# Kernel tuning notes

Hardware: AMD Instinct MI355X
Metric: run time of the kernel (lower is better)

Reference implementation:

```python
import jax, jax.numpy as jnp
import numpy as np

NEG_SLOPE = 0.2  # PyG GATConv default


def setup_inputs() -> dict:
    key = jax.random.key(0)
    k1, k2, k3, k4, k5, k6 = jax.random.split(key, 6)
    N, F_in, F_out, E = 50000, 512, 256, 400000
    x = jax.random.normal(k1, (N, F_in), dtype=jnp.float32)
    adj = jax.random.randint(k2, (2, E), 0, N, dtype=jnp.int64)  # [2, E] edge_index (src, dst)
    glorot = lambda k, shape: jax.random.uniform(
        k, shape, jnp.float32, -1.0, 1.0) * np.sqrt(6.0 / (shape[0] + shape[-1]))
    W = glorot(k3, (F_in, F_out))
    att_src = glorot(k4, (F_out,))
    att_dst = glorot(k5, (F_out,))
    bias = jnp.zeros((F_out,), dtype=jnp.float32)
    return {"x": x, "adj": adj, "W": W, "att_src": att_src, "att_dst": att_dst, "bias": bias}


def reference(x, adj, W, att_src, att_dst, bias):
    N = x.shape[0]
    # add self loops (PyG GATConv default add_self_loops=True)
    loops = jnp.arange(N, dtype=adj.dtype)
    src = jnp.concatenate([adj[0], loops])
    dst = jnp.concatenate([adj[1], loops])

    h = x @ W                          # [N, F_out] projected features
    a_src = h @ att_src                # [N] per-node source attention term
    a_dst = h @ att_dst                # [N]
    e = a_src[src] + a_dst[dst]        # [E+N] edge logits
    e = jnp.where(e > 0, e, NEG_SLOPE * e)  # leaky_relu

    # per-destination softmax over incoming edges (numerically stable)
    m = jax.ops.segment_max(e, dst, num_segments=N)
    ex = jnp.exp(e - m[dst])
    denom = jax.ops.segment_sum(ex, dst, num_segments=N)
    alpha = ex / denom[dst]            # [E+N]

    # weighted scatter-aggregate of source messages
    out = jax.ops.segment_sum(alpha[:, None] * h[src], dst, num_segments=N)
    out = out + bias
    return jax.nn.relu(out)
```

## Files before the change

### kernel.cpp

```cpp
#include <hip/hip_runtime.h>
#include <hip/hip_bf16.h>

typedef __attribute__((ext_vector_type(8))) short bf16x8;
typedef __attribute__((ext_vector_type(4))) float f32x4;
typedef unsigned short u16;

#define F_IN 512
#define F_OUT 256
#define NEG_SLOPE 0.2f
#define LSTRIDE 40

__device__ __forceinline__ float leaky(float e) { return e > 0.f ? e : NEG_SLOPE * e; }

__device__ __forceinline__ u16 f2bf(float x) {
    __hip_bfloat16 h = __float2bfloat16(x);
    return *reinterpret_cast<u16*>(&h);
}
__device__ __forceinline__ void bf2x2(unsigned p, float& a, float& b) {
    a = __uint_as_float(p << 16);
    b = __uint_as_float(p & 0xffff0000u);
}

__device__ __forceinline__ unsigned f2o(float f) {
    unsigned u = __float_as_uint(f);
    return (u & 0x80000000u) ? ~u : (u | 0x80000000u);
}
__device__ __forceinline__ float o2f(unsigned u) {
    return (u & 0x80000000u) ? __uint_as_float(u & 0x7fffffffu) : __uint_as_float(~u);
}

__global__ void k_transpose(const float* __restrict__ W, u16* __restrict__ Wt) {
    int t = blockIdx.x * 256 + threadIdx.x;
    int k = t >> 8;
    int n = t & 255;
    Wt[n * F_IN + k] = f2bf(W[k * F_OUT + n]);
}

__global__ __launch_bounds__(256) void k_gemm(const float* __restrict__ X,
                                              const u16* __restrict__ Wt,
                                              u16* __restrict__ Hb, int N) {
    __shared__ short sA[128 * LSTRIDE];
    __shared__ short sB[128 * LSTRIDE];
    const int tid = threadIdx.x;
    const int wave = tid >> 6, lane = tid & 63;
    const int wm = (wave >> 1) * 64, wn = (wave & 1) * 64;
    const int tile_m = blockIdx.y * 128, tile_n = blockIdx.x * 128;

    f32x4 acc[4][4];
#pragma unroll
    for (int i = 0; i < 4; i++)
#pragma unroll
        for (int j = 0; j < 4; j++) acc[i][j] = (f32x4){0.f, 0.f, 0.f, 0.f};

    const int r0 = tid >> 2;
    const int p0 = tid & 3;

    float4 px[2][2];
    bf16x8 pw[2];

#define ISSUE_LOADS(KB)                                                                 \
    do {                                                                                \
        _Pragma("unroll") for (int j = 0; j < 2; ++j) {                                 \
            int row = r0 + j * 64;                                                      \
            int arow = tile_m + row;                                                    \
            if (arow >= N) arow = N - 1;                                                \
            const float4* xa = (const float4*)&X[(size_t)arow * F_IN + (KB)*32 + p0*8]; \
            px[j][0] = xa[0];                                                           \
            px[j][1] = xa[1];                                                           \
            pw[j] = *(const bf16x8*)&Wt[(size_t)(tile_n + row) * F_IN + (KB)*32 + p0*8];\
        }                                                                               \
    } while (0)

    ISSUE_LOADS(0);

    for (int kb = 0; kb < F_IN / 32; ++kb) {
#pragma unroll
        for (int j = 0; j < 2; ++j) {
            int row = r0 + j * 64;
            u16 s8[8] = {f2bf(px[j][0].x), f2bf(px[j][0].y), f2bf(px[j][0].z), f2bf(px[j][0].w),
                         f2bf(px[j][1].x), f2bf(px[j][1].y), f2bf(px[j][1].z), f2bf(px[j][1].w)};
            *(bf16x8*)&sA[row * LSTRIDE + p0 * 8] = *(const bf16x8*)s8;
            *(bf16x8*)&sB[row * LSTRIDE + p0 * 8] = pw[j];
        }
        __syncthreads();

        if (kb + 1 < F_IN / 32) ISSUE_LOADS(kb + 1);

        const int lm = lane & 15, lk = (lane >> 4) * 8;
        bf16x8 af[4], bfr[4];
#pragma unroll
        for (int i = 0; i < 4; i++) {
            af[i]  = *(const bf16x8*)&sA[(wm + i * 16 + lm) * LSTRIDE + lk];
            bfr[i] = *(const bf16x8*)&sB[(wn + i * 16 + lm) * LSTRIDE + lk];
        }
#pragma unroll
        for (int i = 0; i < 4; i++)
#pragma unroll
            for (int j = 0; j < 4; j++)
                acc[i][j] = __builtin_amdgcn_mfma_f32_16x16x32_bf16(af[i], bfr[j], acc[i][j], 0, 0, 0);
        __syncthreads();
    }
#undef ISSUE_LOADS

    const int lc = lane & 15, lr4 = (lane >> 4) * 4;
    for (int i = 0; i < 4; i++)
        for (int j = 0; j < 4; j++) {
#pragma unroll
            for (int r = 0; r < 4; r++) {
                int row = tile_m + wm + i * 16 + lr4 + r;
                int col = tile_n + wn + j * 16 + lc;
                if (row < N) Hb[(size_t)row * F_OUT + col] = f2bf(acc[i][j][r]);
            }
        }
}

__global__ __launch_bounds__(256) void k_dots(const u16* __restrict__ Hb,
                                              const float* __restrict__ att_src,
                                              const float* __restrict__ att_dst,
                                              float* __restrict__ aS, float* __restrict__ aD,
                                              unsigned* __restrict__ mEnc,
                                              float* __restrict__ denom, int* __restrict__ deg,
                                              int N) {
    int wave = threadIdx.x >> 6, lane = threadIdx.x & 63;
    int row = blockIdx.x * 4 + wave;
    if (row >= N) return;
    uint2 rv = *(const uint2*)&Hb[(size_t)row * F_OUT + lane * 4];
    float h0, h1, h2, h3;
    bf2x2(rv.x, h0, h1);
    bf2x2(rv.y, h2, h3);
    const float4 as = *(const float4*)&att_src[lane * 4];
    const float4 ad = *(const float4*)&att_dst[lane * 4];
    float s1 = h0 * as.x + h1 * as.y + h2 * as.z + h3 * as.w;
    float s2 = h0 * ad.x + h1 * ad.y + h2 * ad.z + h3 * ad.w;
    for (int off = 32; off; off >>= 1) {
        s1 += __shfl_down(s1, off);
        s2 += __shfl_down(s2, off);
    }
    if (lane == 0) {
        aS[row] = s1;
        aD[row] = s2;
        mEnc[row] = f2o(leaky(s1 + s2));
        denom[row] = 0.f;
        deg[row] = 0;
    }
}

__global__ void k_edge_max(const int* __restrict__ srcs, const int* __restrict__ dsts,
                           const float* __restrict__ aS, const float* __restrict__ aD,
                           unsigned* __restrict__ mEnc, int* __restrict__ deg, int E) {
    int e = blockIdx.x * 256 + threadIdx.x;
    if (e >= E) return;
    int s = srcs[e], d = dsts[e];
    float le = leaky(aS[s] + aD[d]);
    atomicMax(&mEnc[d], f2o(le));
    atomicAdd(&deg[d], 1);
}

__global__ __launch_bounds__(256) void k_scan1(const int* __restrict__ deg,
                                               int* __restrict__ bsum, int N) {
    __shared__ int ws[4];
    int t = threadIdx.x;
    int i = blockIdx.x * 256 + t;
    int v = (i < N) ? deg[i] : 0;
    for (int off = 32; off; off >>= 1) v += __shfl_down(v, off);
    if ((t & 63) == 0) ws[t >> 6] = v;
    __syncthreads();
    if (t == 0) bsum[blockIdx.x] = ws[0] + ws[1] + ws[2] + ws[3];
}

__global__ __launch_bounds__(256) void k_scan2(const int* __restrict__ bsum,
                                               int* __restrict__ boff, int* __restrict__ offs,
                                               int nb, int N) {
    __shared__ int ss[256];
    int t = threadIdx.x;
    int v = (t < nb) ? bsum[t] : 0;
    ss[t] = v;
    __syncthreads();
    for (int off = 1; off < 256; off <<= 1) {
        int u = (t >= off) ? ss[t - off] : 0;
        __syncthreads();
        ss[t] += u;
        __syncthreads();
    }
    boff[t] = ss[t] - v;
    if (t == 255) offs[N] = ss[255];
}

__global__ __launch_bounds__(256) void k_scan3(const int* __restrict__ deg,
                                               const int* __restrict__ boff,
                                               int* __restrict__ offs, int* __restrict__ cur,
                                               int N) {
    __shared__ int ss[256];
    int t = threadIdx.x;
    int i = blockIdx.x * 256 + t;
    int v = (i < N) ? deg[i] : 0;
    ss[t] = v;
    __syncthreads();
    for (int off = 1; off < 256; off <<= 1) {
        int u = (t >= off) ? ss[t - off] : 0;
        __syncthreads();
        ss[t] += u;
        __syncthreads();
    }
    int ex = ss[t] - v + boff[blockIdx.x];
    if (i < N) {
        offs[i] = ex;
        cur[i] = ex;
    }
}

__global__ void k_edge_scatter(const int* __restrict__ srcs, const int* __restrict__ dsts,
                               const float* __restrict__ aS, const float* __restrict__ aD,
                               const unsigned* __restrict__ mEnc, float* __restrict__ denom,
                               int* __restrict__ cur, int* __restrict__ csrS,
                               float* __restrict__ csrW, int E) {
    int e = blockIdx.x * 256 + threadIdx.x;
    if (e >= E) return;
    int s = srcs[e], d = dsts[e];
    float le = leaky(aS[s] + aD[d]);
    float ex = __expf(le - o2f(mEnc[d]));
    atomicAdd(&denom[d], ex);
    int pos = atomicAdd(&cur[d], 1);
    csrS[pos] = s;
    csrW[pos] = ex;
}

__global__ __launch_bounds__(256) void k_aggregate(const u16* __restrict__ Hb,
                                                   const float* __restrict__ aS,
                                                   const float* __restrict__ aD,
                                                   const unsigned* __restrict__ mEnc,
                                                   const float* __restrict__ denom,
                                                   const int* __restrict__ offs,
                                                   const int* __restrict__ csrS,
                                                   const float* __restrict__ csrW,
                                                   const float* __restrict__ bias,
                                                   float* __restrict__ out, int N) {
    int wave = threadIdx.x >> 6, lane = threadIdx.x & 63;
    int i = blockIdx.x * 4 + wave;
    if (i >= N) return;
    float mi = o2f(mEnc[i]);
    float sex = __expf(leaky(aS[i] + aD[i]) - mi);
    float inv = 1.f / (denom[i] + sex);

    uint2 rv = *(const uint2*)&Hb[(size_t)i * F_OUT + lane * 4];
    float f0, f1, f2, f3;
    bf2x2(rv.x, f0, f1);
    bf2x2(rv.y, f2, f3);
    float4 acc = {sex * f0, sex * f1, sex * f2, sex * f3};

    int beg = offs[i], end = offs[i + 1];
    int k = beg;
    for (; k + 4 <= end; k += 4) {
        int s0 = csrS[k], s1 = csrS[k + 1], s2 = csrS[k + 2], s3 = csrS[k + 3];
        float w0 = csrW[k], w1 = csrW[k + 1], w2 = csrW[k + 2], w3 = csrW[k + 3];
        uint2 g0 = *(const uint2*)&Hb[(size_t)s0 * F_OUT + lane * 4];
        uint2 g1 = *(const uint2*)&Hb[(size_t)s1 * F_OUT + lane * 4];
        uint2 g2 = *(const uint2*)&Hb[(size_t)s2 * F_OUT + lane * 4];
        uint2 g3 = *(const uint2*)&Hb[(size_t)s3 * F_OUT + lane * 4];
        bf2x2(g0.x, f0, f1); bf2x2(g0.y, f2, f3);
        acc.x += w0 * f0; acc.y += w0 * f1; acc.z += w0 * f2; acc.w += w0 * f3;
        bf2x2(g1.x, f0, f1); bf2x2(g1.y, f2, f3);
        acc.x += w1 * f0; acc.y += w1 * f1; acc.z += w1 * f2; acc.w += w1 * f3;
        bf2x2(g2.x, f0, f1); bf2x2(g2.y, f2, f3);
        acc.x += w2 * f0; acc.y += w2 * f1; acc.z += w2 * f2; acc.w += w2 * f3;
        bf2x2(g3.x, f0, f1); bf2x2(g3.y, f2, f3);
        acc.x += w3 * f0; acc.y += w3 * f1; acc.z += w3 * f2; acc.w += w3 * f3;
    }
    for (; k < end; ++k) {
        int s = csrS[k];
        float w = csrW[k];
        uint2 r = *(const uint2*)&Hb[(size_t)s * F_OUT + lane * 4];
        bf2x2(r.x, f0, f1);
        bf2x2(r.y, f2, f3);
        acc.x += w * f0;
        acc.y += w * f1;
        acc.z += w * f2;
        acc.w += w * f3;
    }
    const float4 bv = *(const float4*)&bias[lane * 4];
    float4 o;
    o.x = acc.x * inv + bv.x;
    o.y = acc.y * inv + bv.y;
    o.z = acc.z * inv + bv.z;
    o.w = acc.w * inv + bv.w;
    o.x = o.x > 0.f ? o.x : 0.f;
    o.y = o.y > 0.f ? o.y : 0.f;
    o.z = o.z > 0.f ? o.z : 0.f;
    o.w = o.w > 0.f ? o.w : 0.f;
    *(float4*)&out[(size_t)i * F_OUT + lane * 4] = o;
}

extern "C" void kernel_launch(void* const* d_in, const int* in_sizes, int n_in,
                              void* d_out, int out_size, void* d_ws, size_t ws_size,
                              hipStream_t stream) {
    const float* X = (const float*)d_in[0];
    const int* adj = (const int*)d_in[1];
    const float* W = (const float*)d_in[2];
    const float* att_src = (const float*)d_in[3];
    const float* att_dst = (const float*)d_in[4];
    const float* bias = (const float*)d_in[5];
    float* out = (float*)d_out;

    const int N = in_sizes[0] / F_IN;
    const int E = in_sizes[1] / 2;
    const int* srcs = adj;
    const int* dsts = adj + E;
    const int nb = (N + 255) / 256;

    char* p = (char*)d_ws;
    auto take = [&](size_t b) -> char* {
        char* q = p;
        p += (b + 255) & ~(size_t)255;
        return q;
    };
    u16* Hb = (u16*)take((size_t)N * F_OUT * sizeof(u16));
    u16* Wt = (u16*)take((size_t)F_IN * F_OUT * sizeof(u16));
    float* aS = (float*)take((size_t)N * sizeof(float));
    float* aD = (float*)take((size_t)N * sizeof(float));
    unsigned* mEnc = (unsigned*)take((size_t)N * sizeof(unsigned));
    float* denom = (float*)take((size_t)N * sizeof(float));
    int* deg = (int*)take((size_t)N * sizeof(int));
    int* offs = (int*)take((size_t)(N + 1) * sizeof(int));
    int* cur = (int*)take((size_t)N * sizeof(int));
    int* bsum = (int*)take((size_t)256 * sizeof(int));
    int* boff = (int*)take((size_t)256 * sizeof(int));
    int* csrS = (int*)take((size_t)E * sizeof(int));
    float* csrW = (float*)take((size_t)E * sizeof(float));

    k_transpose<<<(F_IN * F_OUT) / 256, 256, 0, stream>>>(W, Wt);
    dim3 ggrid((F_OUT + 127) / 128, (N + 127) / 128);
    k_gemm<<<ggrid, 256, 0, stream>>>(X, Wt, Hb, N);
    k_dots<<<(N + 3) / 4, 256, 0, stream>>>(Hb, att_src, att_dst, aS, aD, mEnc, denom, deg, N);
    k_edge_max<<<(E + 255) / 256, 256, 0, stream>>>(srcs, dsts, aS, aD, mEnc, deg, E);
    k_scan1<<<nb, 256, 0, stream>>>(deg, bsum, N);
    k_scan2<<<1, 256, 0, stream>>>(bsum, boff, offs, nb, N);
    k_scan3<<<nb, 256, 0, stream>>>(deg, boff, offs, cur, N);
    k_edge_scatter<<<(E + 255) / 256, 256, 0, stream>>>(srcs, dsts, aS, aD, mEnc, denom, cur,
                                                        csrS, csrW, E);
    k_aggregate<<<(N + 3) / 4, 256, 0, stream>>>(Hb, aS, aD, mEnc, denom, offs, csrS, csrW,
                                                 bias, out, N);
}
```

Before: 328.7 us.

## Drop segment max and denom atomics; use direct-to-LDS loads in GEMM

The softmax no longer subtracts the per-destination max. Unnormalised exp weights are stored in CSR, and each destination's denominator is summed inside the aggregate kernel, which removes the atomicMax pass and the denom atomics. The GEMM now loads fp32 X and bf16 Wt tiles straight into LDS through global_load_lds with XOR-swizzled layouts, and converts to bf16 at fragment-read time. This drops the register-staged prefetch, so global loads no longer overlap with MFMA work, and skipping the max subtraction risks exp overflow for large logits.

Result: faster. 290.8 us (-11.5%).

```diff
diff --git a/kernel.cpp b/kernel.cpp
--- a/kernel.cpp
+++ b/kernel.cpp
@@ -8,7 +8,6 @@
 #define F_IN 512
 #define F_OUT 256
 #define NEG_SLOPE 0.2f
-#define LSTRIDE 40
 
 __device__ __forceinline__ float leaky(float e) { return e > 0.f ? e : NEG_SLOPE * e; }
 
@@ -21,12 +20,9 @@
     b = __uint_as_float(p & 0xffff0000u);
 }
 
-__device__ __forceinline__ unsigned f2o(float f) {
-    unsigned u = __float_as_uint(f);
-    return (u & 0x80000000u) ? ~u : (u | 0x80000000u);
-}
-__device__ __forceinline__ float o2f(unsigned u) {
-    return (u & 0x80000000u) ? __uint_as_float(u & 0x7fffffffu) : __uint_as_float(~u);
+__device__ __forceinline__ void dma16(const void* g, void* l) {
+    __builtin_amdgcn_global_load_lds((const __attribute__((address_space(1))) void*)g,
+                                     (__attribute__((address_space(3))) void*)l, 16, 0, 0);
 }
 
 __global__ void k_transpose(const float* __restrict__ W, u16* __restrict__ Wt) {
@@ -39,8 +35,8 @@
 __global__ __launch_bounds__(256) void k_gemm(const float* __restrict__ X,
                                               const u16* __restrict__ Wt,
                                               u16* __restrict__ Hb, int N) {
-    __shared__ short sA[128 * LSTRIDE];
-    __shared__ short sB[128 * LSTRIDE];
+    __shared__ float sA[128 * 32];
+    __shared__ u16 sB[128 * 32];
     const int tid = threadIdx.x;
     const int wave = tid >> 6, lane = tid & 63;
     const int wm = (wave >> 1) * 64, wn = (wave & 1) * 64;
@@ -52,46 +48,40 @@
 #pragma unroll
         for (int j = 0; j < 4; j++) acc[i][j] = (f32x4){0.f, 0.f, 0.f, 0.f};
 
-    const int r0 = tid >> 2;
-    const int p0 = tid & 3;
-
-    float4 px[2][2];
-    bf16x8 pw[2];
-
-#define ISSUE_LOADS(KB)                                                                 \
-    do {                                                                                \
-        _Pragma("unroll") for (int j = 0; j < 2; ++j) {                                 \
-            int row = r0 + j * 64;                                                      \
-            int arow = tile_m + row;                                                    \
-            if (arow >= N) arow = N - 1;                                                \
-            const float4* xa = (const float4*)&X[(size_t)arow * F_IN + (KB)*32 + p0*8]; \
-            px[j][0] = xa[0];                                                           \
-            px[j][1] = xa[1];                                                           \
-            pw[j] = *(const bf16x8*)&Wt[(size_t)(tile_n + row) * F_IN + (KB)*32 + p0*8];\
-        }                                                                               \
-    } while (0)
-
-    ISSUE_LOADS(0);
+    const int a_row_in = lane >> 3;
+    const int a_gc = (lane & 7) ^ a_row_in;
+    const int b_row_in = lane >> 2;
+    const int b_gc = (lane & 3) ^ ((lane >> 3) & 3);
 
     for (int kb = 0; kb < F_IN / 32; ++kb) {
 #pragma unroll
-        for (int j = 0; j < 2; ++j) {
-            int row = r0 + j * 64;
-            u16 s8[8] = {f2bf(px[j][0].x), f2bf(px[j][0].y), f2bf(px[j][0].z), f2bf(px[j][0].w),
-                         f2bf(px[j][1].x), f2bf(px[j][1].y), f2bf(px[j][1].z), f2bf(px[j][1].w)};
-            *(bf16x8*)&sA[row * LSTRIDE + p0 * 8] = *(const bf16x8*)s8;
-            *(bf16x8*)&sB[row * LSTRIDE + p0 * 8] = pw[j];
+        for (int t = 0; t < 4; ++t) {
+            int r0 = wave * 32 + t * 8;
+            int grow = tile_m + r0 + a_row_in;
+            if (grow >= N) grow = N - 1;
+            dma16(&X[(size_t)grow * F_IN + kb * 32 + a_gc * 4], &sA[r0 * 32]);
         }
-        __syncthreads();
-
-        if (kb + 1 < F_IN / 32) ISSUE_LOADS(kb + 1);
-
-        const int lm = lane & 15, lk = (lane >> 4) * 8;
+#pragma unroll
+        for (int t = 0; t < 2; ++t) {
+            int r0 = wave * 32 + t * 16;
+            int grow = tile_n + r0 + b_row_in;
+            dma16(&Wt[(size_t)grow * F_IN + kb * 32 + b_gc * 8], &sB[r0 * 32]);
+        }
+        __syncthreads();
+
+        const int lm = lane & 15, q = lane >> 4;
         bf16x8 af[4], bfr[4];
 #pragma unroll
         for (int i = 0; i < 4; i++) {
-            af[i]  = *(const bf16x8*)&sA[(wm + i * 16 + lm) * LSTRIDE + lk];
-            bfr[i] = *(const bf16x8*)&sB[(wn + i * 16 + lm) * LSTRIDE + lk];
+            const int arow = wm + i * 16 + lm;
+            const int s7 = arow & 7;
+            const float4 c0 = *(const float4*)&sA[arow * 32 + (((2 * q) ^ s7) << 2)];
+            const float4 c1 = *(const float4*)&sA[arow * 32 + (((2 * q + 1) ^ s7) << 2)];
+            u16 a8[8] = {f2bf(c0.x), f2bf(c0.y), f2bf(c0.z), f2bf(c0.w),
+                         f2bf(c1.x), f2bf(c1.y), f2bf(c1.z), f2bf(c1.w)};
+            af[i] = *(const bf16x8*)a8;
+            const int brow = wn + i * 16 + lm;
+            bfr[i] = *(const bf16x8*)&sB[brow * 32 + ((q ^ ((lm >> 1) & 3)) << 3)];
         }
 #pragma unroll
         for (int i = 0; i < 4; i++)
@@ -100,7 +90,6 @@
                 acc[i][j] = __builtin_amdgcn_mfma_f32_16x16x32_bf16(af[i], bfr[j], acc[i][j], 0, 0, 0);
         __syncthreads();
     }
-#undef ISSUE_LOADS
 
     const int lc = lane & 15, lr4 = (lane >> 4) * 4;
     for (int i = 0; i < 4; i++)
@@ -118,9 +107,7 @@
                                               const float* __restrict__ att_src,
                                               const float* __restrict__ att_dst,
                                               float* __restrict__ aS, float* __restrict__ aD,
-                                              unsigned* __restrict__ mEnc,
-                                              float* __restrict__ denom, int* __restrict__ deg,
-                                              int N) {
+                                              int* __restrict__ deg, int N) {
     int wave = threadIdx.x >> 6, lane = threadIdx.x & 63;
     int row = blockIdx.x * 4 + wave;
     if (row >= N) return;
@@ -139,21 +126,14 @@
     if (lane == 0) {
         aS[row] = s1;
         aD[row] = s2;
-        mEnc[row] = f2o(leaky(s1 + s2));
-        denom[row] = 0.f;
         deg[row] = 0;
     }
 }
 
-__global__ void k_edge_max(const int* __restrict__ srcs, const int* __restrict__ dsts,
-                           const float* __restrict__ aS, const float* __restrict__ aD,
-                           unsigned* __restrict__ mEnc, int* __restrict__ deg, int E) {
+__global__ void k_deg(const int* __restrict__ dsts, int* __restrict__ deg, int E) {
     int e = blockIdx.x * 256 + threadIdx.x;
     if (e >= E) return;
-    int s = srcs[e], d = dsts[e];
-    float le = leaky(aS[s] + aD[d]);
-    atomicMax(&mEnc[d], f2o(le));
-    atomicAdd(&deg[d], 1);
+    atomicAdd(&deg[dsts[e]], 1);
 }
 
 __global__ __launch_bounds__(256) void k_scan1(const int* __restrict__ deg,
@@ -211,15 +191,12 @@
 
 __global__ void k_edge_scatter(const int* __restrict__ srcs, const int* __restrict__ dsts,
                                const float* __restrict__ aS, const float* __restrict__ aD,
-                               const unsigned* __restrict__ mEnc, float* __restrict__ denom,
                                int* __restrict__ cur, int* __restrict__ csrS,
                                float* __restrict__ csrW, int E) {
     int e = blockIdx.x * 256 + threadIdx.x;
     if (e >= E) return;
     int s = srcs[e], d = dsts[e];
-    float le = leaky(aS[s] + aD[d]);
-    float ex = __expf(le - o2f(mEnc[d]));
-    atomicAdd(&denom[d], ex);
+    float ex = __expf(leaky(aS[s] + aD[d]));
     int pos = atomicAdd(&cur[d], 1);
     csrS[pos] = s;
     csrW[pos] = ex;
@@ -228,8 +205,6 @@
 __global__ __launch_bounds__(256) void k_aggregate(const u16* __restrict__ Hb,
                                                    const float* __restrict__ aS,
                                                    const float* __restrict__ aD,
-                                                   const unsigned* __restrict__ mEnc,
-                                                   const float* __restrict__ denom,
                                                    const int* __restrict__ offs,
                                                    const int* __restrict__ csrS,
                                                    const float* __restrict__ csrW,
@@ -238,15 +213,14 @@
     int wave = threadIdx.x >> 6, lane = threadIdx.x & 63;
     int i = blockIdx.x * 4 + wave;
     if (i >= N) return;
-    float mi = o2f(mEnc[i]);
-    float sex = __expf(leaky(aS[i] + aD[i]) - mi);
-    float inv = 1.f / (denom[i] + sex);
+    float sex = __expf(leaky(aS[i] + aD[i]));
 
     uint2 rv = *(const uint2*)&Hb[(size_t)i * F_OUT + lane * 4];
     float f0, f1, f2, f3;
     bf2x2(rv.x, f0, f1);
     bf2x2(rv.y, f2, f3);
     float4 acc = {sex * f0, sex * f1, sex * f2, sex * f3};
+    float wsum = sex;
 
     int beg = offs[i], end = offs[i + 1];
     int k = beg;
@@ -257,6 +231,7 @@
         uint2 g1 = *(const uint2*)&Hb[(size_t)s1 * F_OUT + lane * 4];
         uint2 g2 = *(const uint2*)&Hb[(size_t)s2 * F_OUT + lane * 4];
         uint2 g3 = *(const uint2*)&Hb[(size_t)s3 * F_OUT + lane * 4];
+        wsum += w0 + w1 + w2 + w3;
         bf2x2(g0.x, f0, f1); bf2x2(g0.y, f2, f3);
         acc.x += w0 * f0; acc.y += w0 * f1; acc.z += w0 * f2; acc.w += w0 * f3;
         bf2x2(g1.x, f0, f1); bf2x2(g1.y, f2, f3);
@@ -270,6 +245,7 @@
         int s = csrS[k];
         float w = csrW[k];
         uint2 r = *(const uint2*)&Hb[(size_t)s * F_OUT + lane * 4];
+        wsum += w;
         bf2x2(r.x, f0, f1);
         bf2x2(r.y, f2, f3);
         acc.x += w * f0;
@@ -277,6 +253,7 @@
         acc.z += w * f2;
         acc.w += w * f3;
     }
+    float inv = 1.f / wsum;
     const float4 bv = *(const float4*)&bias[lane * 4];
     float4 o;
     o.x = acc.x * inv + bv.x;
@@ -317,8 +294,6 @@
     u16* Wt = (u16*)take((size_t)F_IN * F_OUT * sizeof(u16));
     float* aS = (float*)take((size_t)N * sizeof(float));
     float* aD = (float*)take((size_t)N * sizeof(float));
-    unsigned* mEnc = (unsigned*)take((size_t)N * sizeof(unsigned));
-    float* denom = (float*)take((size_t)N * sizeof(float));
     int* deg = (int*)take((size_t)N * sizeof(int));
     int* offs = (int*)take((size_t)(N + 1) * sizeof(int));
     int* cur = (int*)take((size_t)N * sizeof(int));
@@ -330,13 +305,11 @@
     k_transpose<<<(F_IN * F_OUT) / 256, 256, 0, stream>>>(W, Wt);
     dim3 ggrid((F_OUT + 127) / 128, (N + 127) / 128);
     k_gemm<<<ggrid, 256, 0, stream>>>(X, Wt, Hb, N);
-    k_dots<<<(N + 3) / 4, 256, 0, stream>>>(Hb, att_src, att_dst, aS, aD, mEnc, denom, deg, N);
-    k_edge_max<<<(E + 255) / 256, 256, 0, stream>>>(srcs, dsts, aS, aD, mEnc, deg, E);
+    k_dots<<<(N + 3) / 4, 256, 0, stream>>>(Hb, att_src, att_dst, aS, aD, deg, N);
+    k_deg<<<(E + 255) / 256, 256, 0, stream>>>(dsts, deg, E);
     k_scan1<<<nb, 256, 0, stream>>>(deg, bsum, N);
     k_scan2<<<1, 256, 0, stream>>>(bsum, boff, offs, nb, N);
     k_scan3<<<nb, 256, 0, stream>>>(deg, boff, offs, cur, N);
-    k_edge_scatter<<<(E + 255) / 256, 256, 0, stream>>>(srcs, dsts, aS, aD, mEnc, denom, cur,
-                                                        csrS, csrW, E);
-    k_aggregate<<<(N + 3) / 4, 256, 0, stream>>>(Hb, aS, aD, mEnc, denom, offs, csrS, csrW,
-                                                 bias, out, N);
-}
+    k_edge_scatter<<<(E + 255) / 256, 256, 0, stream>>>(srcs, dsts, aS, aD, cur, csrS, csrW, E);
+    k_aggregate<<<(N + 3) / 4, 256, 0, stream>>>(Hb, aS, aD, offs, csrS, csrW, bias, out, N);
+}
```
